# Performance work log

Measured on AMD Instinct MI355X. Metric: run time of the kernel, lower is better.

Reference implementation:

```python
import jax, jax.numpy as jnp
import numpy as np

B, N, E = 4, 4096, 2048
H_DIM = 2048
HEADS = 16
DH = H_DIM // HEADS
LN_EPS = 1e-5


def setup_inputs() -> dict:
    key = jax.random.key(0)
    ks = jax.random.split(key, 10)
    s = 1.0 / np.sqrt(E)
    so = 1.0 / np.sqrt(H_DIM)
    return {
        "x": jax.random.normal(ks[0], (B, N, E), jnp.float32),
        "Wqk": jax.random.normal(ks[1], (E, H_DIM), jnp.float32) * s,
        "bqk": jnp.zeros((H_DIM,), jnp.float32),
        "Wv": jax.random.normal(ks[2], (E, H_DIM), jnp.float32) * s,
        "bv": jnp.zeros((H_DIM,), jnp.float32),
        "Wu": jax.random.normal(ks[3], (E, H_DIM), jnp.float32) * s,
        "bu": jnp.zeros((H_DIM,), jnp.float32),
        "Wo": jax.random.normal(ks[4], (H_DIM, E), jnp.float32) * so,
        "bo": jnp.zeros((E,), jnp.float32),
        "ln_g": jnp.ones((H_DIM,), jnp.float32),
        "ln_b": jnp.zeros((H_DIM,), jnp.float32),
    }


def _heads(t):
    # [b, n, (h d)] -> [b, h, n, d]
    b, n, _ = t.shape
    return t.reshape(b, n, HEADS, DH).transpose(0, 2, 1, 3)


def _layernorm(x, g, b):
    mu = jnp.mean(x, axis=-1, keepdims=True)
    var = jnp.mean(jnp.square(x - mu), axis=-1, keepdims=True)
    return (x - mu) * jax.lax.rsqrt(var + LN_EPS) * g + b


def reference(x, Wqk, bqk, Wv, bv, Wu, bu, Wo, bo, ln_g, ln_b):
    # y = x (self-attention); qk_proj shared for q and k
    q = x @ Wqk + bqk
    k = x @ Wqk + bqk
    v = jax.nn.silu(x @ Wv + bv)   # uv_act = swish
    u = jax.nn.silu(x @ Wu + bu)
    q = jax.nn.elu(_heads(q))      # act = elu (applied after head split)
    kh = jax.nn.elu(_heads(k))
    vh = _heads(v)
    # non-causal associative form: kv = k^T v, out = q @ kv
    kv = jnp.einsum('bhnd,bhne->bhde', kh, vh)
    out = jnp.einsum('bhnd,bhde->bhne', q, kv)
    out = out.transpose(0, 2, 1, 3).reshape(x.shape[0], x.shape[1], H_DIM)
    out = _layernorm(out, ln_g, ln_b)
    out = u * out
    return out @ Wo + bo
```

## Files before the change

kernel.cpp:

```cpp
#include <hip/hip_runtime.h>

typedef __attribute__((ext_vector_type(8))) short short8;
typedef __attribute__((ext_vector_type(4))) float floatx4;

__device__ __forceinline__ float b2f(unsigned short u) {
  union { unsigned int i; float f; } c; c.i = ((unsigned int)u) << 16; return c.f;
}
__device__ __forceinline__ unsigned short f2b(float f) {
  union { float f; unsigned int i; } c; c.f = f;
  unsigned int i = c.i;
  return (unsigned short)((i + 0x7FFFu + ((i >> 16) & 1u)) >> 16);
}
__device__ __forceinline__ float elu_f(float x) {
  return x > 0.f ? x : (expf(x) - 1.f);
}
__device__ __forceinline__ float silu_f(float x) {
  return x / (1.f + expf(-x));
}
__device__ __forceinline__ void async16(const unsigned short* g, unsigned short* l) {
  __builtin_amdgcn_global_load_lds(
      (const __attribute__((address_space(1))) void*)g,
      (__attribute__((address_space(3))) void*)l, 16, 0, 0);
}
__device__ __forceinline__ floatx4 mfma16(short8 a, short8 b, floatx4 c) {
  return __builtin_amdgcn_mfma_f32_16x16x32_bf16(a, b, c, 0, 0, 0);
}

__global__ __launch_bounds__(256) void detect_dtype(
    const unsigned int* __restrict__ x, int* __restrict__ cnt) {
  int t = threadIdx.x;
  int c = 0;
  for (int i = t; i < 4096; i += 256) {
    unsigned int lo = x[i] & 0xFFFFu;
    unsigned int e = (lo >> 7) & 0xFFu;
    if (e >= 0x70u && e <= 0x8Fu) c++;
  }
#pragma unroll
  for (int off = 32; off > 0; off >>= 1) c += __shfl_down(c, off, 64);
  if ((t & 63) == 0) atomicAdd(cnt, c);
}
__device__ __forceinline__ bool is_f32(const int* flag) { return flag[0] < 2048; }

__global__ __launch_bounds__(256) void convert_x(
    const void* __restrict__ x, unsigned short* __restrict__ xb,
    const int* __restrict__ flag) {
  if (!is_f32(flag)) return;
  size_t i = ((size_t)blockIdx.x * 256 + threadIdx.x) * 8;
  const float* xf = (const float*)x;
  float4 a = *(const float4*)(xf + i);
  float4 b = *(const float4*)(xf + i + 4);
  unsigned short p[8] = {f2b(a.x), f2b(a.y), f2b(a.z), f2b(a.w),
                         f2b(b.x), f2b(b.y), f2b(b.z), f2b(b.w)};
  *(uint4*)(xb + i) = *(uint4*)p;
}

__global__ __launch_bounds__(256) void transpose2048(
    const void* __restrict__ src, unsigned short* __restrict__ dst,
    const int* __restrict__ flag) {
  const bool f32 = is_f32(flag);
  __shared__ unsigned short tile[32][33];
  int bx = blockIdx.x * 32;
  int by = blockIdx.y * 32;
  int tx = threadIdx.x & 31;
  int ty = threadIdx.x >> 5;
  for (int i = ty; i < 32; i += 8) {
    size_t idx = (size_t)(by + i) * 2048 + bx + tx;
    tile[i][tx] = f32 ? f2b(((const float*)src)[idx]) : ((const unsigned short*)src)[idx];
  }
  __syncthreads();
  for (int i = ty; i < 32; i += 8)
    dst[(size_t)(bx + i) * 2048 + by + tx] = tile[tx][i];
}

__global__ __launch_bounds__(512, 2) void gemm256(
    const unsigned short* __restrict__ A0,
    const unsigned short* __restrict__ A1, int a_sel,
    const unsigned short* __restrict__ WT,
    const void* __restrict__ bias,
    void* __restrict__ C, int c_ext,
    int K, int Nc, int act, const int* __restrict__ flag) {
  const bool f32 = is_f32(flag);
  const unsigned short* A = (a_sel && f32) ? A1 : A0;
  __shared__ __align__(16) unsigned short lds[8 * 8192];
#define CH(b, m, ks) (lds + ((((b)*2 + (m)) * 2 + (ks)) * 8192))
  const int bn = blockIdx.x * 256;
  const int bm = blockIdx.y * 256;
  const int t = threadIdx.x;
  const int lane = t & 63;
  const int wave = t >> 6;
  const int lm = lane & 15;
  const int quad = lane >> 4;
  const int wm = (wave >> 2) * 128;
  const int wn = (wave & 3) * 64;
  const int srow = lane >> 2;
  const int scol = (lane & 3) * 8;
  const int NT = K >> 6;

  floatx4 acc[8][4] = {};

  auto stageA = [&](int kt, int ks, unsigned short* ch) {
#pragma unroll
    for (int c = 0; c < 2; ++c) {
      int rr = c * 128 + wave * 16;
      async16(A + (size_t)(bm + rr + srow) * K + kt + ks * 32 + scol, ch + rr * 32);
    }
  };
  auto stageB = [&](int kt, int ks, unsigned short* ch) {
#pragma unroll
    for (int c = 0; c < 2; ++c) {
      int rr = c * 128 + wave * 16;
      async16(WT + (size_t)(bn + rr + srow) * K + kt + ks * 32 + scol, ch + rr * 32);
    }
  };

  stageA(0, 0, CH(0, 0, 0));
  stageB(0, 0, CH(0, 1, 0));
  stageA(0, 1, CH(0, 0, 1));
  stageB(0, 1, CH(0, 1, 1));
  asm volatile("s_waitcnt vmcnt(4)" ::: "memory");
  asm volatile("s_barrier" ::: "memory");

  for (int ti = 0; ti < NT; ++ti) {
    const int buf = ti & 1, nb = buf ^ 1;
    const int ktn = (ti + 1 < NT ? ti + 1 : ti) << 6;
    const unsigned short* cA0 = CH(buf, 0, 0);
    const unsigned short* cB0 = CH(buf, 1, 0);
    const unsigned short* cA1 = CH(buf, 0, 1);
    const unsigned short* cB1 = CH(buf, 1, 1);
    short8 af[8], bf0, bf1;

#pragma unroll
    for (int mi = 0; mi < 8; ++mi)
      af[mi] = *(const short8*)(cA0 + (wm + mi * 16 + lm) * 32 + quad * 8);
    bf0 = *(const short8*)(cB0 + (wn + lm) * 32 + quad * 8);
    bf1 = *(const short8*)(cB0 + (wn + 16 + lm) * 32 + quad * 8);
    stageA(ktn, 0, CH(nb, 0, 0));
    asm volatile("s_barrier" ::: "memory");
    asm volatile("s_waitcnt lgkmcnt(0)" ::: "memory");
    __builtin_amdgcn_sched_barrier(0);
    __builtin_amdgcn_s_setprio(1);
#pragma unroll
    for (int mi = 0; mi < 8; ++mi) {
      acc[mi][0] = mfma16(af[mi], bf0, acc[mi][0]);
      acc[mi][1] = mfma16(af[mi], bf1, acc[mi][1]);
    }
    __builtin_amdgcn_s_setprio(0);
    asm volatile("s_barrier" ::: "memory");

    bf0 = *(const short8*)(cB0 + (wn + 32 + lm) * 32 + quad * 8);
    bf1 = *(const short8*)(cB0 + (wn + 48 + lm) * 32 + quad * 8);
    stageB(ktn, 0, CH(nb, 1, 0));
    asm volatile("s_barrier" ::: "memory");
    asm volatile("s_waitcnt lgkmcnt(0)" ::: "memory");
    __builtin_amdgcn_sched_barrier(0);
    __builtin_amdgcn_s_setprio(1);
#pragma unroll
    for (int mi = 0; mi < 8; ++mi) {
      acc[mi][2] = mfma16(af[mi], bf0, acc[mi][2]);
      acc[mi][3] = mfma16(af[mi], bf1, acc[mi][3]);
    }
    __builtin_amdgcn_s_setprio(0);
    asm volatile("s_waitcnt vmcnt(4)" ::: "memory");
    asm volatile("s_barrier" ::: "memory");

#pragma unroll
    for (int mi = 0; mi < 8; ++mi)
      af[mi] = *(const short8*)(cA1 + (wm + mi * 16 + lm) * 32 + quad * 8);
    bf0 = *(const short8*)(cB1 + (wn + lm) * 32 + quad * 8);
    bf1 = *(const short8*)(cB1 + (wn + 16 + lm) * 32 + quad * 8);
    stageA(ktn, 1, CH(nb, 0, 1));
    asm volatile("s_barrier" ::: "memory");
    asm volatile("s_waitcnt lgkmcnt(0)" ::: "memory");
    __builtin_amdgcn_sched_barrier(0);
    __builtin_amdgcn_s_setprio(1);
#pragma unroll
    for (int mi = 0; mi < 8; ++mi) {
      acc[mi][0] = mfma16(af[mi], bf0, acc[mi][0]);
      acc[mi][1] = mfma16(af[mi], bf1, acc[mi][1]);
    }
    __builtin_amdgcn_s_setprio(0);
    asm volatile("s_barrier" ::: "memory");

    bf0 = *(const short8*)(cB1 + (wn + 32 + lm) * 32 + quad * 8);
    bf1 = *(const short8*)(cB1 + (wn + 48 + lm) * 32 + quad * 8);
    stageB(ktn, 1, CH(nb, 1, 1));
    asm volatile("s_barrier" ::: "memory");
    asm volatile("s_waitcnt lgkmcnt(0)" ::: "memory");
    __builtin_amdgcn_sched_barrier(0);
    __builtin_amdgcn_s_setprio(1);
#pragma unroll
    for (int mi = 0; mi < 8; ++mi) {
      acc[mi][2] = mfma16(af[mi], bf0, acc[mi][2]);
      acc[mi][3] = mfma16(af[mi], bf1, acc[mi][3]);
    }
    __builtin_amdgcn_s_setprio(0);
    asm volatile("s_waitcnt vmcnt(4)" ::: "memory");
    asm volatile("s_barrier" ::: "memory");
  }
  asm volatile("s_waitcnt vmcnt(0)" ::: "memory");

#pragma unroll
  for (int ni = 0; ni < 4; ++ni) {
    int col = bn + wn + ni * 16 + lm;
    float bv = f32 ? ((const float*)bias)[col] : b2f(((const unsigned short*)bias)[col]);
#pragma unroll
    for (int mi = 0; mi < 8; ++mi) {
#pragma unroll
      for (int r = 0; r < 4; ++r) {
        int row = bm + wm + mi * 16 + quad * 4 + r;
        float v = acc[mi][ni][r] + bv;
        if (act == 1) v = silu_f(v);
        size_t idx = (size_t)row * Nc + col;
        if (c_ext && f32) ((float*)C)[idx] = v;
        else ((unsigned short*)C)[idx] = f2b(v);
      }
    }
  }
#undef CH
}

__global__ __launch_bounds__(256) void kv_accum(
    const unsigned short* __restrict__ QK,
    const unsigned short* __restrict__ V,
    float* __restrict__ kvT, int chunk) {
  const int bh = blockIdx.x;
  const int sp = blockIdx.y;
  const int b = bh >> 4, h = bh & 15;
  __shared__ __align__(16) unsigned short Kt[128][72];
  __shared__ __align__(16) unsigned short Vt[128][72];
  const int t = threadIdx.x;
  const int lane = t & 63, wave = t >> 6;
  const int lm = lane & 15, quad = lane >> 4;
  const int wm = (wave >> 1) * 64, wn = (wave & 1) * 64;
  floatx4 acc[4][4] = {};
  const size_t base = (size_t)b * 4096 * 2048 + (size_t)h * 128;
  const int nl = t & 63;
  const int dg0 = t >> 6;
  for (int n0 = sp * chunk; n0 < (sp + 1) * chunk; n0 += 64) {
#pragma unroll
    for (int i = 0; i < 4; ++i) {
      int dg = dg0 + 4 * i;
      union { uint4 u; unsigned short s[8]; } vk, vv;
      vk.u = *(const uint4*)(QK + base + (size_t)(n0 + nl) * 2048 + dg * 8);
      vv.u = *(const uint4*)(V + base + (size_t)(n0 + nl) * 2048 + dg * 8);
#pragma unroll
      for (int j = 0; j < 8; ++j) {
        Kt[dg * 8 + j][nl] = f2b(elu_f(b2f(vk.s[j])));
        Vt[dg * 8 + j][nl] = vv.s[j];
      }
    }
    __syncthreads();
#pragma unroll
    for (int ks = 0; ks < 2; ++ks) {
      short8 af[4], bf[4];
#pragma unroll
      for (int mi = 0; mi < 4; ++mi)
        af[mi] = *(const short8*)&Kt[wm + mi * 16 + lm][ks * 32 + quad * 8];
#pragma unroll
      for (int ni = 0; ni < 4; ++ni)
        bf[ni] = *(const short8*)&Vt[wn + ni * 16 + lm][ks * 32 + quad * 8];
#pragma unroll
      for (int mi = 0; mi < 4; ++mi)
#pragma unroll
        for (int ni = 0; ni < 4; ++ni)
          acc[mi][ni] = __builtin_amdgcn_mfma_f32_16x16x32_bf16(
              af[mi], bf[ni], acc[mi][ni], 0, 0, 0);
    }
    __syncthreads();
  }
  float* dst = kvT + (size_t)bh * 128 * 128;
#pragma unroll
  for (int mi = 0; mi < 4; ++mi)
#pragma unroll
    for (int ni = 0; ni < 4; ++ni)
#pragma unroll
      for (int r = 0; r < 4; ++r) {
        int d = wm + mi * 16 + quad * 4 + r;
        int e = wn + ni * 16 + lm;
        atomicAdd(&dst[e * 128 + d], acc[mi][ni][r]);
      }
}

__global__ __launch_bounds__(256) void attn_out(
    const unsigned short* __restrict__ QK,
    const float* __restrict__ kvT,
    unsigned short* __restrict__ O) {
  const int h = blockIdx.x;
  const int bm = blockIdx.y * 128;
  const int b = bm >> 12;
  const int bh = b * 16 + h;
  __shared__ __align__(16) unsigned short As[128][136];
  __shared__ __align__(16) unsigned short Bs[128][136];
  const int t = threadIdx.x;
  const int lane = t & 63, wave = t >> 6;
  const int lm = lane & 15, quad = lane >> 4;
  const int wm = (wave >> 1) * 64, wn = (wave & 1) * 64;
  {
    const int r0 = t >> 4;
    const int g = t & 15;
#pragma unroll
    for (int i = 0; i < 8; ++i) {
      int r = r0 + 16 * i;
      union { uint4 u; unsigned short s[8]; } vq, w;
      vq.u = *(const uint4*)(QK + (size_t)(bm + r) * 2048 + h * 128 + g * 8);
#pragma unroll
      for (int j = 0; j < 8; ++j) w.s[j] = f2b(elu_f(b2f(vq.s[j])));
      *(uint4*)&As[r][g * 8] = w.u;
    }
    const int e0 = t >> 5;
    const int gg = t & 31;
    const float* kvp = kvT + (size_t)bh * 16384;
#pragma unroll
    for (int i = 0; i < 16; ++i) {
      int e = e0 + 8 * i;
      float4 f = *(const float4*)(kvp + e * 128 + gg * 4);
      unsigned short o4[4] = {f2b(f.x), f2b(f.y), f2b(f.z), f2b(f.w)};
      *(uint2*)&Bs[e][gg * 4] = *(uint2*)o4;
    }
  }
  __syncthreads();
  floatx4 acc[4][4] = {};
#pragma unroll
  for (int ks = 0; ks < 4; ++ks) {
    short8 af[4], bf[4];
#pragma unroll
    for (int mi = 0; mi < 4; ++mi)
      af[mi] = *(const short8*)&As[wm + mi * 16 + lm][ks * 32 + quad * 8];
#pragma unroll
    for (int ni = 0; ni < 4; ++ni)
      bf[ni] = *(const short8*)&Bs[wn + ni * 16 + lm][ks * 32 + quad * 8];
#pragma unroll
    for (int mi = 0; mi < 4; ++mi)
#pragma unroll
      for (int ni = 0; ni < 4; ++ni)
        acc[mi][ni] = __builtin_amdgcn_mfma_f32_16x16x32_bf16(
            af[mi], bf[ni], acc[mi][ni], 0, 0, 0);
  }
#pragma unroll
  for (int mi = 0; mi < 4; ++mi)
#pragma unroll
    for (int ni = 0; ni < 4; ++ni)
#pragma unroll
      for (int r = 0; r < 4; ++r) {
        int row = bm + wm + mi * 16 + quad * 4 + r;
        int e = wn + ni * 16 + lm;
        O[(size_t)row * 2048 + h * 128 + e] = f2b(acc[mi][ni][r]);
      }
}

__global__ __launch_bounds__(256) void ln_mul(
    const unsigned short* __restrict__ O,
    const unsigned short* __restrict__ U,
    const void* __restrict__ g,
    const void* __restrict__ bb,
    unsigned short* __restrict__ T, const int* __restrict__ flag) {
  const bool f32 = is_f32(flag);
  const int row = blockIdx.x;
  const int t = threadIdx.x;
  const unsigned short* o = O + (size_t)row * 2048;
  float vals[8];
  float s = 0.f, s2 = 0.f;
#pragma unroll
  for (int i = 0; i < 8; ++i) {
    float f = b2f(o[t + 256 * i]);
    vals[i] = f;
    s += f;
    s2 += f * f;
  }
#pragma unroll
  for (int off = 32; off > 0; off >>= 1) {
    s += __shfl_down(s, off, 64);
    s2 += __shfl_down(s2, off, 64);
  }
  __shared__ float ps[4], ps2[4];
  int lane = t & 63, wave = t >> 6;
  if (lane == 0) { ps[wave] = s; ps2[wave] = s2; }
  __syncthreads();
  float S = ps[0] + ps[1] + ps[2] + ps[3];
  float S2 = ps2[0] + ps2[1] + ps2[2] + ps2[3];
  float mu = S * (1.f / 2048.f);
  float var = S2 * (1.f / 2048.f) - mu * mu;
  float rs = rsqrtf(var + 1e-5f);
#pragma unroll
  for (int i = 0; i < 8; ++i) {
    int c = t + 256 * i;
    float gv = f32 ? ((const float*)g)[c] : b2f(((const unsigned short*)g)[c]);
    float bv = f32 ? ((const float*)bb)[c] : b2f(((const unsigned short*)bb)[c]);
    float nv = (vals[i] - mu) * rs * gv + bv;
    float uu = b2f(U[(size_t)row * 2048 + c]);
    T[(size_t)row * 2048 + c] = f2b(nv * uu);
  }
}

extern "C" void kernel_launch(void* const* d_in, const int* in_sizes, int n_in,
                              void* d_out, int out_size, void* d_ws, size_t ws_size,
                              hipStream_t stream) {
  const void* x   = d_in[0];
  const void* Wqk = d_in[1];
  const void* bqk = d_in[2];
  const void* Wv  = d_in[3];
  const void* bv  = d_in[4];
  const void* Wu  = d_in[5];
  const void* bu  = d_in[6];
  const void* Wo  = d_in[7];
  const void* bo  = d_in[8];
  const void* lng = d_in[9];
  const void* lnb = d_in[10];

  char* ws = (char*)d_ws;
  const size_t MB = 1024 * 1024;
  int* flag = (int*)ws;
  unsigned short* WT   = (unsigned short*)(ws + 1 * MB);
  unsigned short* buf0 = (unsigned short*)(ws + 16 * MB);
  unsigned short* buf1 = (unsigned short*)(ws + 80 * MB);
  float* kvT = (float*)(ws + 144 * MB);
  unsigned short* xb = (unsigned short*)(ws + 148 * MB);

  dim3 tb(256);
  dim3 gb(512);
  dim3 ggrid(8, 64);
  hipMemsetAsync(flag, 0, 4096, stream);
  hipMemsetAsync(kvT, 0, (size_t)64 * 128 * 128 * 4, stream);
  detect_dtype<<<1, tb, 0, stream>>>((const unsigned int*)x, flag);
  convert_x<<<16384, tb, 0, stream>>>(x, xb, flag);

  const unsigned short* xs = (const unsigned short*)x;
  transpose2048<<<dim3(64, 64), tb, 0, stream>>>(Wqk, WT, flag);
  gemm256<<<ggrid, gb, 0, stream>>>(xs, xb, 1, WT, bqk, buf0, 0, 2048, 2048, 0, flag);
  transpose2048<<<dim3(64, 64), tb, 0, stream>>>(Wv, WT, flag);
  gemm256<<<ggrid, gb, 0, stream>>>(xs, xb, 1, WT, bv, buf1, 0, 2048, 2048, 1, flag);
  kv_accum<<<dim3(64, 8), tb, 0, stream>>>(buf0, buf1, kvT, 512);
  attn_out<<<dim3(16, 128), tb, 0, stream>>>(buf0, kvT, buf1);
  transpose2048<<<dim3(64, 64), tb, 0, stream>>>(Wu, WT, flag);
  gemm256<<<ggrid, gb, 0, stream>>>(xs, xb, 1, WT, bu, buf0, 0, 2048, 2048, 1, flag);
  ln_mul<<<16384, tb, 0, stream>>>(buf1, buf0, lng, lnb, buf1, flag);
  transpose2048<<<dim3(64, 64), tb, 0, stream>>>(Wo, WT, flag);
  gemm256<<<ggrid, gb, 0, stream>>>(buf1, buf1, 0, WT, bo, d_out, 1, 2048, 2048, 0, flag);
}
```

Baseline: 1.125 ms.

## Swizzle GEMM LDS layout and remap workgroups across XCDs

Applies an XOR swizzle to the LDS column chunk used by the async global-to-LDS loads and the matching fragment reads in the 256x256 GEMM. The goal is to cut LDS bank conflicts on the short8 reads. It also remaps the flat workgroup index so that consecutive tiles land on the same XCD (an 8-way round-robin remap) in both gemm256 and attn_out, to improve L2 locality. The remap assumes the workgroup count is divisible by 8.

Result: faster. 1.084 ms (-3.7%).

```diff
diff --git a/kernel.cpp b/kernel.cpp
--- a/kernel.cpp
+++ b/kernel.cpp
@@ -83,8 +83,13 @@
   const unsigned short* A = (a_sel && f32) ? A1 : A0;
   __shared__ __align__(16) unsigned short lds[8 * 8192];
 #define CH(b, m, ks) (lds + ((((b)*2 + (m)) * 2 + (ks)) * 8192))
-  const int bn = blockIdx.x * 256;
-  const int bm = blockIdx.y * 256;
+  const int nbx = gridDim.x;
+  const int flat = blockIdx.y * nbx + blockIdx.x;
+  const int nwg = nbx * gridDim.y;
+  const int cpx = nwg >> 3;
+  const int nf = (flat & 7) * cpx + (flat >> 3);
+  const int bn = (nf % nbx) * 256;
+  const int bm = (nf / nbx) * 256;
   const int t = threadIdx.x;
   const int lane = t & 63;
   const int wave = t >> 6;
@@ -93,7 +98,8 @@
   const int wm = (wave >> 2) * 128;
   const int wn = (wave & 3) * 64;
   const int srow = lane >> 2;
-  const int scol = (lane & 3) * 8;
+  const int scol = (((lane & 3) ^ ((lane >> 3) & 3)) * 8);
+  const int rq = (quad ^ ((lm >> 1) & 3)) * 8;
   const int NT = K >> 6;
 
   floatx4 acc[8][4] = {};
@@ -131,9 +137,9 @@
 
 #pragma unroll
     for (int mi = 0; mi < 8; ++mi)
-      af[mi] = *(const short8*)(cA0 + (wm + mi * 16 + lm) * 32 + quad * 8);
-    bf0 = *(const short8*)(cB0 + (wn + lm) * 32 + quad * 8);
-    bf1 = *(const short8*)(cB0 + (wn + 16 + lm) * 32 + quad * 8);
+      af[mi] = *(const short8*)(cA0 + (wm + mi * 16 + lm) * 32 + rq);
+    bf0 = *(const short8*)(cB0 + (wn + lm) * 32 + rq);
+    bf1 = *(const short8*)(cB0 + (wn + 16 + lm) * 32 + rq);
     stageA(ktn, 0, CH(nb, 0, 0));
     asm volatile("s_barrier" ::: "memory");
     asm volatile("s_waitcnt lgkmcnt(0)" ::: "memory");
@@ -147,8 +153,8 @@
     __builtin_amdgcn_s_setprio(0);
     asm volatile("s_barrier" ::: "memory");
 
-    bf0 = *(const short8*)(cB0 + (wn + 32 + lm) * 32 + quad * 8);
-    bf1 = *(const short8*)(cB0 + (wn + 48 + lm) * 32 + quad * 8);
+    bf0 = *(const short8*)(cB0 + (wn + 32 + lm) * 32 + rq);
+    bf1 = *(const short8*)(cB0 + (wn + 48 + lm) * 32 + rq);
     stageB(ktn, 0, CH(nb, 1, 0));
     asm volatile("s_barrier" ::: "memory");
     asm volatile("s_waitcnt lgkmcnt(0)" ::: "memory");
@@ -165,9 +171,9 @@
 
 #pragma unroll
     for (int mi = 0; mi < 8; ++mi)
-      af[mi] = *(const short8*)(cA1 + (wm + mi * 16 + lm) * 32 + quad * 8);
-    bf0 = *(const short8*)(cB1 + (wn + lm) * 32 + quad * 8);
-    bf1 = *(const short8*)(cB1 + (wn + 16 + lm) * 32 + quad * 8);
+      af[mi] = *(const short8*)(cA1 + (wm + mi * 16 + lm) * 32 + rq);
+    bf0 = *(const short8*)(cB1 + (wn + lm) * 32 + rq);
+    bf1 = *(const short8*)(cB1 + (wn + 16 + lm) * 32 + rq);
     stageA(ktn, 1, CH(nb, 0, 1));
     asm volatile("s_barrier" ::: "memory");
     asm volatile("s_waitcnt lgkmcnt(0)" ::: "memory");
@@ -181,8 +187,8 @@
     __builtin_amdgcn_s_setprio(0);
     asm volatile("s_barrier" ::: "memory");
 
-    bf0 = *(const short8*)(cB1 + (wn + 32 + lm) * 32 + quad * 8);
-    bf1 = *(const short8*)(cB1 + (wn + 48 + lm) * 32 + quad * 8);
+    bf0 = *(const short8*)(cB1 + (wn + 32 + lm) * 32 + rq);
+    bf1 = *(const short8*)(cB1 + (wn + 48 + lm) * 32 + rq);
     stageB(ktn, 1, CH(nb, 1, 1));
     asm volatile("s_barrier" ::: "memory");
     asm volatile("s_waitcnt lgkmcnt(0)" ::: "memory");
@@ -285,8 +291,10 @@
     const unsigned short* __restrict__ QK,
     const float* __restrict__ kvT,
     unsigned short* __restrict__ O) {
-  const int h = blockIdx.x;
-  const int bm = blockIdx.y * 128;
+  const int flat0 = blockIdx.y * 16 + blockIdx.x;
+  const int nf = (flat0 & 7) * 256 + (flat0 >> 3);
+  const int h = nf & 15;
+  const int bm = (nf >> 4) * 128;
   const int b = bm >> 12;
   const int bh = b * 16 + h;
   __shared__ __align__(16) unsigned short As[128][136];
```
